# Kernel optimization log

Hardware: AMD Instinct MI355X
Metric: run time of the kernel (lower is better)

Reference implementation:

```python
import jax, jax.numpy as jnp
import numpy as np

HID = 256
HEADS = 4
NUM_GRAPHS = 8
NUM_RISK = 6

def _lstm_dir(x_pre, whh):
    # x_pre: [L, 4H] (input proj + both biases folded in), whh: [4H, H]
    Hh = whh.shape[1]
    def step(carry, xp):
        h, c = carry
        g = xp + whh @ h
        i, f, gg, o = jnp.split(g, 4)
        c = jax.nn.sigmoid(f) * c + jax.nn.sigmoid(i) * jnp.tanh(gg)
        h = jax.nn.sigmoid(o) * jnp.tanh(c)
        return (h, c), h
    init = (jnp.zeros((Hh,), x_pre.dtype), jnp.zeros((Hh,), x_pre.dtype))
    _, hs = jax.lax.scan(step, init, x_pre)
    return hs

def bilstm(x, wif, whf, bif, bhf, wir, whr, bir, bhr):
    pre_f = x @ wif.T + bif + bhf
    pre_r = x @ wir.T + bir + bhr
    hf = _lstm_dir(pre_f, whf)
    hb = _lstm_dir(pre_r[::-1], whr)[::-1]
    return jnp.concatenate([hf, hb], axis=-1)  # [N, 2H]

def gcn(h, src, dst, w, b, n):
    # PyG GCNConv: add self loops, symmetric deg^{-1/2} normalization
    xw = h @ w.T
    loop = jnp.arange(n, dtype=src.dtype)
    s = jnp.concatenate([src, loop]); d = jnp.concatenate([dst, loop])
    deg = jax.ops.segment_sum(jnp.ones_like(s, dtype=xw.dtype), d, num_segments=n)
    dinv = jax.lax.rsqrt(deg)  # deg >= 1 due to self loops
    coef = (dinv[s] * dinv[d])[:, None]
    return jax.ops.segment_sum(xw[s] * coef, d, num_segments=n) + b

def mha(h, in_w, in_b, out_w, out_b):
    # unbatched torch nn.MultiheadAttention, h: [L, E]
    L, E = h.shape
    hd = E // HEADS
    q, k, v = jnp.split(h @ in_w.T + in_b, 3, axis=-1)
    sp = lambda t: t.reshape(L, HEADS, hd).transpose(1, 0, 2)  # [H, L, hd]
    q, k, v = sp(q), sp(k), sp(v)
    a = jax.nn.softmax(jnp.einsum('hld,hmd->hlm', q, k) / np.sqrt(hd).astype(np.float32), axis=-1)
    o = jnp.einsum('hlm,hmd->hld', a, v).transpose(1, 0, 2).reshape(L, E)
    return o @ out_w.T + out_b

def ln(x, g, b, eps=1e-5):
    m = x.mean(-1, keepdims=True)
    v = ((x - m) ** 2).mean(-1, keepdims=True)
    return (x - m) * jax.lax.rsqrt(v + eps) * g + b

def setup_inputs() -> dict:
    key = jax.random.key(0)
    ks = iter(jax.random.split(key, 48))
    def nrm(shape, s=0.02):
        return jax.random.normal(next(ks), shape, dtype=jnp.float32) * s
    N, D, E, B, C, H = 3072, 768, 49152, NUM_GRAPHS, NUM_RISK, HID
    inp = {}
    inp['x'] = jax.random.normal(next(ks), (N, D), dtype=jnp.float32)
    inp['edge_index'] = jax.random.randint(next(ks), (2, E), 0, N, dtype=jnp.int32)
    inp['batch'] = jnp.sort(jax.random.randint(next(ks), (N,), 0, B, dtype=jnp.int32))
    # bidirectional LSTM (torch gate order i,f,g,o)
    inp['lstm_wif'] = nrm((4 * H, D)); inp['lstm_whf'] = nrm((4 * H, H))
    inp['lstm_bif'] = nrm((4 * H,));   inp['lstm_bhf'] = nrm((4 * H,))
    inp['lstm_wir'] = nrm((4 * H, D)); inp['lstm_whr'] = nrm((4 * H, H))
    inp['lstm_bir'] = nrm((4 * H,));   inp['lstm_bhr'] = nrm((4 * H,))
    # GCN layers (conv3 exists but is unused in forward)
    inp['gcn1_w'] = nrm((H, 2 * H)); inp['gcn1_b'] = nrm((H,))
    inp['gcn2_w'] = nrm((H, H));     inp['gcn2_b'] = nrm((H,))
    # per-risk-category attention / gate / predictor, stacked over C=6
    inp['attn_in_w'] = nrm((C, 3 * H, H)); inp['attn_in_b'] = nrm((C, 3 * H))
    inp['attn_out_w'] = nrm((C, H, H));    inp['attn_out_b'] = nrm((C, H))
    inp['gate_w1'] = nrm((C, H, 2 * H)); inp['gate_b1'] = nrm((C, H))
    inp['gate_w2'] = nrm((C, 1, H));     inp['gate_b2'] = nrm((C, 1))
    inp['pred_w1'] = nrm((C, 64, H)); inp['pred_b1'] = nrm((C, 64))
    inp['pred_w2'] = nrm((C, 1, 64)); inp['pred_b2'] = nrm((C, 1))
    # 2-layer post-LN TransformerEncoder, d_model=256, nhead=4, d_ff=2048
    inp['tr_in_w'] = nrm((2, 3 * H, H)); inp['tr_in_b'] = nrm((2, 3 * H))
    inp['tr_out_w'] = nrm((2, H, H));    inp['tr_out_b'] = nrm((2, H))
    inp['tr_ff1_w'] = nrm((2, 2048, H)); inp['tr_ff1_b'] = nrm((2, 2048))
    inp['tr_ff2_w'] = nrm((2, H, 2048)); inp['tr_ff2_b'] = nrm((2, H))
    inp['tr_ln1_g'] = jnp.ones((2, H), jnp.float32); inp['tr_ln1_b'] = nrm((2, H))
    inp['tr_ln2_g'] = jnp.ones((2, H), jnp.float32); inp['tr_ln2_b'] = nrm((2, H))
    return inp

def reference(x, edge_index, batch,
              lstm_wif, lstm_whf, lstm_bif, lstm_bhf,
              lstm_wir, lstm_whr, lstm_bir, lstm_bhr,
              gcn1_w, gcn1_b, gcn2_w, gcn2_b,
              attn_in_w, attn_in_b, attn_out_w, attn_out_b,
              gate_w1, gate_b1, gate_w2, gate_b2,
              pred_w1, pred_b1, pred_w2, pred_b2,
              tr_in_w, tr_in_b, tr_out_w, tr_out_b,
              tr_ff1_w, tr_ff1_b, tr_ff2_w, tr_ff2_b,
              tr_ln1_g, tr_ln1_b, tr_ln2_g, tr_ln2_b):
    N = x.shape[0]
    B = NUM_GRAPHS
    h = bilstm(x, lstm_wif, lstm_whf, lstm_bif, lstm_bhf,
               lstm_wir, lstm_whr, lstm_bir, lstm_bhr)  # [N, 512]
    src, dst = edge_index[0], edge_index[1]
    h = jax.nn.relu(gcn(h, src, dst, gcn1_w, gcn1_b, N))  # dropout is identity in eval
    h = jax.nn.relu(gcn(h, src, dst, gcn2_w, gcn2_b, N))  # [N, 256]
    counts = jnp.clip(jax.ops.segment_sum(jnp.ones((N,), h.dtype), batch, num_segments=B), 1.0)[:, None]
    scores, pooled_list = [], []
    for i in range(NUM_RISK):
        att = mha(h, attn_in_w[i], attn_in_b[i], attn_out_w[i], attn_out_b[i])
        g = jax.nn.sigmoid(jax.nn.relu(jnp.concatenate([h, att], -1) @ gate_w1[i].T + gate_b1[i]) @ gate_w2[i].T + gate_b2[i])
        prop = h + g * att
        pooled = jax.ops.segment_sum(prop, batch, num_segments=B) / counts  # [B, 256]
        sc = jax.nn.sigmoid(jax.nn.relu(pooled @ pred_w1[i].T + pred_b1[i]) @ pred_w2[i].T + pred_b2[i])
        scores.append(sc)
        pooled_list.append(pooled)
    s = jnp.stack(pooled_list, axis=1)  # [B, 6, 256]: torch treats axis0=seq, axis1=batch
    mha_b = jax.vmap(mha, in_axes=(1, None, None, None, None), out_axes=1)
    for l in range(2):  # post-LN TransformerEncoderLayer
        sa = mha_b(s, tr_in_w[l], tr_in_b[l], tr_out_w[l], tr_out_b[l])
        s = ln(s + sa, tr_ln1_g[l], tr_ln1_b[l])
        ff = jax.nn.relu(s @ tr_ff1_w[l].T + tr_ff1_b[l]) @ tr_ff2_w[l].T + tr_ff2_b[l]
        s = ln(s + ff, tr_ln2_g[l], tr_ln2_b[l])
    factor = jax.nn.sigmoid(s.mean(-1, keepdims=True))  # [B, 6, 1]
    out = jnp.stack([scores[i] * (1.0 + 0.2 * factor[:, i, :]) for i in range(NUM_RISK)], axis=0)
    return out  # [6, B, 1]
```

## Files before the change

kernel.cpp:

```cpp
#include <hip/hip_runtime.h>
#include <stdint.h>

typedef unsigned short u16;
typedef unsigned int   u32;
typedef __bf16    bf16x8 __attribute__((ext_vector_type(8)));
typedef float     f32x4  __attribute__((ext_vector_type(4)));
typedef _Float16  f16x2  __attribute__((ext_vector_type(2)));

#define DEV __device__ __forceinline__
#define MFMA16(a,b,c) __builtin_amdgcn_mfma_f32_16x16x32_bf16((a),(b),(c),0,0,0)
#define FDOT2(w,h,a) __builtin_amdgcn_fdot2(__builtin_bit_cast(f16x2,(w)), __builtin_bit_cast(f16x2,(h)), (a), false)

DEV u16  f2bf(float f){ u32 u = __builtin_bit_cast(u32,f); u32 r = (u + 0x7FFFu + ((u>>16)&1u))>>16; return (u16)r; }
DEV float bf2f(u16 b){ u32 u = ((u32)b)<<16; return __builtin_bit_cast(float,u); }
DEV u32  pkf16(float a, float b){ f16x2 p; p.x=(_Float16)a; p.y=(_Float16)b; return __builtin_bit_cast(u32,p); }
DEV u32  pkbf(float a, float b){ u32 r; asm("v_cvt_pk_bf16_f32 %0, %1, %2" : "=v"(r) : "v"(a), "v"(b)); return r; }
DEV float sigm(float x){ return 1.f/(1.f + exp2f(-1.44269504f*x)); }
DEV float tanh_(float x){ x = fminf(fmaxf(x,-15.f),15.f); float e = exp2f(2.88539008f*x); return (e-1.f)/(e+1.f); }

DEV void gl16(const u16* g, u16* l){
  __builtin_amdgcn_global_load_lds((const __attribute__((address_space(1))) void*)g,
                                   (__attribute__((address_space(3))) void*)l, 16, 0, 0);
}

__global__ void k_setup(int* cnt, int* fill, int* bstart, int* bend,
                        float* bias_pre, const float* bif, const float* bhf,
                        const float* bir, const float* bhr, float* pacc){
  int i = blockIdx.x*blockDim.x + threadIdx.x;
  if (i < 3072){ cnt[i]=0; fill[i]=0; }
  if (i < 1024){ bias_pre[i] = bif[i]+bhf[i]; bias_pre[1024+i] = bir[i]+bhr[i]; }
  if (i < 8){ bstart[i]=0; bend[i]=0; }
  if (i < 12288) pacc[i] = 0.f;
}

struct Cvt { const float* s[8]; u16* d[8]; int n[8]; };
__global__ void k_convert(Cvt c){
  for (int seg=0; seg<8; seg++){
    int n4 = c.n[seg]>>2;
    for (int i = blockIdx.x*blockDim.x+threadIdx.x; i < n4; i += gridDim.x*blockDim.x){
      float4 v = ((const float4*)c.s[seg])[i];
      uint2 o; o.x = (u32)f2bf(v.x) | ((u32)f2bf(v.y)<<16);
      o.y = (u32)f2bf(v.z) | ((u32)f2bf(v.w)<<16);
      *(uint2*)(c.d[seg] + (size_t)i*4) = o;
    }
  }
}

template<bool BF16OUT, bool RELU>
__global__ __launch_bounds__(256) void k_gemm(
  const u16* __restrict__ A, const u16* __restrict__ A2, const u16* __restrict__ B,
  const float* __restrict__ bias, void* __restrict__ Cout,
  int M, int N, int K1, int K2,
  long long sA, long long sA2, long long sB, long long sBias, long long sC)
{
  __shared__ __align__(16) u16 lA[128*32];
  __shared__ __align__(16) u16 lB[128*32];
  int bm = blockIdx.x, bn = blockIdx.y, bz = blockIdx.z;
  int tid = threadIdx.x, w = tid>>6, lane = tid&63;
  int wm = w&1, wn = w>>1;
  int m15 = lane&15, q = lane>>4;
  int srow = tid>>2, scol = (tid&3)*8;
  int K = K1+K2;
  f32x4 acc[4][4] = {};
  const u16* Ab  = A + (long long)bz*sA;
  const u16* A2b = A2 ? (A2 + (long long)bz*sA2) : (const u16*)0;
  const u16* Bb  = B + (long long)bz*sB;
  for (int k0 = 0; k0 < K; k0 += 32){
    uint4 av0, av1, bv0, bv1;
    if (k0 < K1){
      av0 = *(const uint4*)(Ab + (long long)(bm*128+srow   )*K1 + k0 + scol);
      av1 = *(const uint4*)(Ab + (long long)(bm*128+srow+64)*K1 + k0 + scol);
    } else {
      av0 = *(const uint4*)(A2b + (long long)(bm*128+srow   )*K2 + (k0-K1) + scol);
      av1 = *(const uint4*)(A2b + (long long)(bm*128+srow+64)*K2 + (k0-K1) + scol);
    }
    bv0 = *(const uint4*)(Bb + (long long)(bn*128+srow   )*K + k0 + scol);
    bv1 = *(const uint4*)(Bb + (long long)(bn*128+srow+64)*K + k0 + scol);
    __syncthreads();
    *(uint4*)&lA[(srow   )*32 + scol] = av0;
    *(uint4*)&lA[(srow+64)*32 + scol] = av1;
    *(uint4*)&lB[(srow   )*32 + scol] = bv0;
    *(uint4*)&lB[(srow+64)*32 + scol] = bv1;
    __syncthreads();
    bf16x8 af[4], bf[4];
    #pragma unroll
    for (int i=0;i<4;i++) af[i] = *(const bf16x8*)&lA[(wm*64+i*16+m15)*32 + q*8];
    #pragma unroll
    for (int j=0;j<4;j++) bf[j] = *(const bf16x8*)&lB[(wn*64+j*16+m15)*32 + q*8];
    #pragma unroll
    for (int i=0;i<4;i++){
      #pragma unroll
      for (int j=0;j<4;j++) acc[i][j] = MFMA16(af[i], bf[j], acc[i][j]);
    }
  }
  #pragma unroll
  for (int j=0;j<4;j++){
    int n = bn*128 + wn*64 + j*16 + m15;
    float bvv = bias ? bias[bz*sBias + n] : 0.f;
    #pragma unroll
    for (int i=0;i<4;i++){
      #pragma unroll
      for (int r=0;r<4;r++){
        int m = bm*128 + wm*64 + i*16 + q*4 + r;
        float v = acc[i][j][r] + bvv;
        if (RELU) v = fmaxf(v, 0.f);
        long long idx = (long long)bz*sC + (long long)m*N + n;
        if (BF16OUT) ((u16*)Cout)[idx] = f2bf(v);
        else         ((float*)Cout)[idx] = v;
      }
    }
  }
}

#define LSEG 24
#define LWARM 48
__global__ __launch_bounds__(512)
void k_lstm(
  const float* __restrict__ pre_all,
  const float* __restrict__ whf, const float* __restrict__ whr,
  u16* __restrict__ h_out)
{
  int bid = blockIdx.x;
  int dir = bid & 1, chunk = bid >> 1;
  int t = threadIdx.x;
  int d0 = t, d1 = t + 512;
  const float* pre = pre_all + (size_t)dir*3072*1024;
  const float* whh = dir ? whr : whf;

  __shared__ __align__(16) u32 wl[1024*28];
  __shared__ __align__(16) u32 hp[128];
  __shared__ float acts_f[256], acts_o[256];
  __shared__ float harr[256];

  u32 wr0[100], wr1[100];
  {
    const float* r0 = whh + (size_t)d0*256;
    const float* r1 = whh + (size_t)d1*256;
    #pragma unroll
    for (int p=0;p<50;p++){
      float4 w4 = *(const float4*)(r0 + 4*p);
      wr0[2*p]   = pkf16(w4.x, w4.y);
      wr0[2*p+1] = pkf16(w4.z, w4.w);
    }
    #pragma unroll
    for (int p=0;p<50;p++){
      float4 w4 = *(const float4*)(r1 + 4*p);
      wr1[2*p]   = pkf16(w4.x, w4.y);
      wr1[2*p+1] = pkf16(w4.z, w4.w);
    }
    #pragma unroll
    for (int p=0;p<14;p++){
      float4 w4 = *(const float4*)(r0 + 200 + 4*p);
      wl[d0*28 + 2*p]   = pkf16(w4.x, w4.y);
      wl[d0*28 + 2*p+1] = pkf16(w4.z, w4.w);
      float4 v4 = *(const float4*)(r1 + 200 + 4*p);
      wl[d1*28 + 2*p]   = pkf16(v4.x, v4.y);
      wl[d1*28 + 2*p+1] = pkf16(v4.z, v4.w);
    }
  }
  if (t < 128) hp[t] = 0u;
  __syncthreads();

  float c = 0.f;
  int warm = min(chunk*LSEG, LWARM);
  int nsteps = warm + LSEG;
  int s0 = chunk*LSEG - warm;
  const uint4* hp4 = (const uint4*)hp;
  const uint4* wl0 = (const uint4*)&wl[d0*28];
  const uint4* wl1 = (const uint4*)&wl[d1*28];
  for (int it = 0; it < nsteps; it++){
    int s = s0 + it;
    int n = dir ? (3071 - s) : s;
    float pv0 = pre[(size_t)n*1024 + d0];
    float pv1 = pre[(size_t)n*1024 + d1];
    float a00=0.f,a01=0.f,a10=0.f,a11=0.f;
    #pragma unroll
    for (int j=0;j<25;j++){
      uint4 h4 = hp4[j];
      a00 = FDOT2(wr0[4*j+0], h4.x, a00);
      a01 = FDOT2(wr0[4*j+1], h4.y, a01);
      a00 = FDOT2(wr0[4*j+2], h4.z, a00);
      a01 = FDOT2(wr0[4*j+3], h4.w, a01);
      a10 = FDOT2(wr1[4*j+0], h4.x, a10);
      a11 = FDOT2(wr1[4*j+1], h4.y, a11);
      a10 = FDOT2(wr1[4*j+2], h4.z, a10);
      a11 = FDOT2(wr1[4*j+3], h4.w, a11);
      __builtin_amdgcn_sched_barrier(0);
    }
    #pragma unroll
    for (int j=0;j<7;j++){
      uint4 h4 = hp4[25+j];
      uint4 w0 = wl0[j];
      uint4 w1 = wl1[j];
      a00 = FDOT2(w0.x, h4.x, a00);
      a01 = FDOT2(w0.y, h4.y, a01);
      a00 = FDOT2(w0.z, h4.z, a00);
      a01 = FDOT2(w0.w, h4.w, a01);
      a10 = FDOT2(w1.x, h4.x, a10);
      a11 = FDOT2(w1.y, h4.y, a11);
      a10 = FDOT2(w1.z, h4.z, a10);
      a11 = FDOT2(w1.w, h4.w, a11);
      __builtin_amdgcn_sched_barrier(0);
    }
    float gv0 = a00 + a01 + pv0;
    float gv1 = a10 + a11 + pv1;
    if (t >= 256){ acts_f[t-256] = sigm(gv0); acts_o[t-256] = sigm(gv1); }
    __syncthreads();
    if (t < 256){
      float ai = sigm(gv0), ag = tanh_(gv1);
      c = acts_f[t]*c + ai*ag;
      harr[t] = acts_o[t]*tanh_(c);
    }
    __syncthreads();
    if (t < 128){
      float h0 = harr[2*t], h1 = harr[2*t+1];
      hp[t] = pkf16(h0, h1);
      if (it >= warm){
        u32 pb = (u32)f2bf(h0) | ((u32)f2bf(h1) << 16);
        *(u32*)&h_out[(size_t)n*512 + dir*256 + 2*t] = pb;
      }
    }
    __syncthreads();
  }
}

__global__ void k_edge_cnt(const int* __restrict__ dst, int* __restrict__ cnt){
  int i = blockIdx.x*blockDim.x + threadIdx.x;
  if (i < 49152) atomicAdd(&cnt[dst[i]], 1);
}
__global__ __launch_bounds__(1024) void k_scan(const int* __restrict__ cnt, int* __restrict__ rowptr, float* __restrict__ dinv){
  __shared__ int lds[1024];
  int t = threadIdx.x;
  int a0 = cnt[t*3], a1 = cnt[t*3+1], a2 = cnt[t*3+2];
  int s = a0+a1+a2;
  lds[t] = s; __syncthreads();
  for (int off=1; off<1024; off<<=1){
    int v = (t>=off) ? lds[t-off] : 0; __syncthreads();
    lds[t] += v; __syncthreads();
  }
  int base = lds[t] - s;
  rowptr[t*3] = base; rowptr[t*3+1] = base+a0; rowptr[t*3+2] = base+a0+a1;
  if (t == 1023) rowptr[3072] = base + s;
  dinv[t*3]   = rsqrtf((float)(a0+1));
  dinv[t*3+1] = rsqrtf((float)(a1+1));
  dinv[t*3+2] = rsqrtf((float)(a2+1));
}
__global__ void k_fill(const int* __restrict__ src, const int* __restrict__ dst,
                       const int* __restrict__ rowptr, int* __restrict__ fill, int* __restrict__ csrc){
  int i = blockIdx.x*blockDim.x + threadIdx.x;
  if (i < 49152){ int d = dst[i]; int pos = rowptr[d] + atomicAdd(&fill[d],1); csrc[pos] = src[i]; }
}

__global__ __launch_bounds__(256) void k_gcn_agg(const float* __restrict__ xw, const int* __restrict__ rowptr,
  const int* __restrict__ csrc, const float* __restrict__ dinv, const float* __restrict__ bias,
  float* __restrict__ outf, u16* __restrict__ outb){
  int wv = threadIdx.x>>6, lane = threadIdx.x&63;
  int dst = blockIdx.x*4 + wv;
  float dd = dinv[dst];
  int beg = rowptr[dst], end = rowptr[dst+1];
  const float4* x4 = (const float4*)xw;
  float4 acc = {0.f,0.f,0.f,0.f};
  for (int e=beg;e<end;e++){
    int s = csrc[e];
    float cf = dd*dinv[s];
    float4 v = x4[(size_t)s*64 + lane];
    acc.x += cf*v.x; acc.y += cf*v.y; acc.z += cf*v.z; acc.w += cf*v.w;
  }
  { float cf = dd*dd; float4 v = x4[(size_t)dst*64+lane];
    acc.x += cf*v.x; acc.y += cf*v.y; acc.z += cf*v.z; acc.w += cf*v.w; }
  float4 bb = ((const float4*)bias)[lane];
  acc.x = fmaxf(acc.x+bb.x,0.f); acc.y = fmaxf(acc.y+bb.y,0.f);
  acc.z = fmaxf(acc.z+bb.z,0.f); acc.w = fmaxf(acc.w+bb.w,0.f);
  if (outf) ((float4*)outf)[(size_t)dst*64+lane] = acc;
  uint2 o; o.x = (u32)f2bf(acc.x) | ((u32)f2bf(acc.y)<<16);
  o.y = (u32)f2bf(acc.z) | ((u32)f2bf(acc.w)<<16);
  *(uint2*)&outb[(size_t)dst*256 + lane*4] = o;
}

__global__ void k_bounds(const int* __restrict__ batch, int* __restrict__ bstart, int* __restrict__ bend){
  int n = blockIdx.x*blockDim.x+threadIdx.x;
  if (n>=3072) return;
  int b = batch[n];
  if (n==0 || batch[n-1]!=b) bstart[b]=n;
  if (n==3071 || batch[n+1]!=b) bend[b]=n+1;
}

__global__ __launch_bounds__(256) void k_vt(const u16* __restrict__ qkv, u16* __restrict__ vT){
  int p = blockIdx.x, nt = blockIdx.y;
  int risk = p >> 2, hd = p & 3;
  __shared__ u16 t[64][72];
  int r = threadIdx.x >> 2, ch = threadIdx.x & 3;
  const u16* src = qkv + (size_t)risk*3072*768 + (size_t)(nt*64 + r)*768 + 512 + hd*64 + ch*16;
  uint4 v0 = *(const uint4*)src;
  uint4 v1 = *(const uint4*)(src+8);
  *(uint4*)&t[r][ch*16] = v0; *(uint4*)&t[r][ch*16+8] = v1;
  __syncthreads();
  int d = threadIdx.x >> 2, nc = threadIdx.x & 3;
  u16 tmp[16];
  #pragma unroll
  for (int j=0;j<16;j++) tmp[j] = t[nc*16 + j][d];
  u32 a0 = (u32)tmp[0] | ((u32)tmp[1]<<16), a1 = (u32)tmp[2] | ((u32)tmp[3]<<16);
  u32 a2 = (u32)tmp[4] | ((u32)tmp[5]<<16), a3 = (u32)tmp[6] | ((u32)tmp[7]<<16);
  u32 a4 = (u32)tmp[8] | ((u32)tmp[9]<<16), a5 = (u32)tmp[10]| ((u32)tmp[11]<<16);
  u32 a6 = (u32)tmp[12]| ((u32)tmp[13]<<16),a7 = (u32)tmp[14]| ((u32)tmp[15]<<16);
  u16* dstp = vT + (size_t)p*64*3072 + (size_t)d*3072 + nt*64 + nc*16;
  uint4 o1 = {a0,a1,a2,a3}; uint4 o2 = {a4,a5,a6,a7};
  *(uint4*)dstp = o1; *(uint4*)(dstp+8) = o2;
}

#define KSW(r,c) (((r)<<6) + ((((c)^((r)&7)))<<3))
__global__ __launch_bounds__(256) void k_flash(const u16* __restrict__ qkv, const u16* __restrict__ vT,
                                               u16* __restrict__ outO){
  int qt = blockIdx.x;
  int pair = blockIdx.y;
  int risk = pair>>2, hd = pair&3;
  int tid = threadIdx.x, w = tid>>6, lane = tid&63;
  int m = lane&15, q = lane>>4;
  __shared__ __align__(16) u16 lK[2][64*64];
  __shared__ __align__(16) u16 lV[2][64*64];
  __shared__ __align__(16) u16 lP[4*16*72];
  const size_t qbase = (size_t)risk*3072*768;
  bf16x8 aq0, aq1;
  {
    const u16* qp = qkv + qbase + (size_t)(qt*64 + w*16 + m)*768 + hd*64 + q*8;
    aq0 = *(const bf16x8*)qp; aq1 = *(const bf16x8*)(qp+32);
  }
  f32x4 o[4] = {};
  f32x4 lrow = {};
  const u16* kg = qkv + qbase + 256 + hd*64;
  const u16* vg = vT + (size_t)pair*64*3072;
  int sro = lane>>3;
  int sch = (lane&7) ^ sro;
  int wbase = w*16*72;
  const float SC = 0.18033688f;
  #pragma unroll
  for (int i=0;i<2;i++){
    int row = w*16 + i*8 + sro;
    gl16(kg + (size_t)row*768 + sch*8,  &lK[0][(w*16+i*8)*64]);
    gl16(vg + (size_t)row*3072 + sch*8, &lV[0][(w*16+i*8)*64]);
  }
  __syncthreads();
  int cur = 0;
  for (int kt=0; kt<48; kt++){
    if (kt < 47){
      int nb = cur^1;
      #pragma unroll
      for (int i=0;i<2;i++){
        int row = w*16 + i*8 + sro;
        gl16(kg + (size_t)((kt+1)*64 + row)*768 + sch*8,   &lK[nb][(w*16+i*8)*64]);
        gl16(vg + (size_t)row*3072 + (kt+1)*64 + sch*8,    &lV[nb][(w*16+i*8)*64]);
      }
    }
    #pragma unroll
    for (int j=0;j<4;j++){
      bf16x8 b0 = *(const bf16x8*)&lK[cur][KSW(j*16+m, q)];
      bf16x8 b1 = *(const bf16x8*)&lK[cur][KSW(j*16+m, q+4)];
      f32x4 cfr = {};
      cfr = MFMA16(aq0, b0, cfr);
      cfr = MFMA16(aq1, b1, cfr);
      float pe[4];
      #pragma unroll
      for (int r=0;r<4;r++){
        pe[r] = exp2f(cfr[r]*SC);
        lrow[r] += pe[r];
      }
      #pragma unroll
      for (int r=0;r<4;r++){
        float po = __shfl_xor(pe[r],1);
        if (!(lane&1)){
          *(u32*)&lP[wbase + (q*4+r)*72 + j*16 + m] = pkbf(pe[r], po);
        }
      }
    }
    bf16x8 ap0 = *(const bf16x8*)&lP[wbase + m*72 + q*8];
    bf16x8 ap1 = *(const bf16x8*)&lP[wbase + m*72 + 32 + q*8];
    #pragma unroll
    for (int jd=0;jd<4;jd++){
      bf16x8 b0 = *(const bf16x8*)&lV[cur][KSW(jd*16+m, q)];
      bf16x8 b1 = *(const bf16x8*)&lV[cur][KSW(jd*16+m, q+4)];
      o[jd] = MFMA16(ap0, b0, o[jd]);
      o[jd] = MFMA16(ap1, b1, o[jd]);
    }
    __syncthreads();
    cur ^= 1;
  }
  float rl[4];
  #pragma unroll
  for (int r=0;r<4;r++){
    float s = lrow[r];
    #pragma unroll
    for (int sh=1; sh<16; sh<<=1) s += __shfl_xor(s, sh);
    rl[r] = 1.f/s;
  }
  #pragma unroll
  for (int jd=0;jd<4;jd++){
    #pragma unroll
    for (int r=0;r<4;r++){
      float v = o[jd][r]*rl[r];
      float vo = __shfl_xor(v,1);
      if (!(lane&1)){
        int row = qt*64 + w*16 + q*4 + r;
        *(u32*)&outO[((size_t)risk*3072 + row)*256 + hd*64 + jd*16 + m] = pkbf(v, vo);
      }
    }
  }
}

__global__ __launch_bounds__(256) void k_gate2(const u16* __restrict__ gh, const float* __restrict__ w2,
    const float* __restrict__ b2, float* __restrict__ g){
  int wv = threadIdx.x>>6, lane = threadIdx.x&63;
  int row = blockIdx.x*4 + wv;
  int i = row / 3072;
  const u16* rp = gh + (size_t)row*256 + lane*4;
  uint2 d = *(const uint2*)rp;
  float4 wv4 = *(const float4*)(w2 + i*256 + lane*4);
  float p = bf2f((u16)(d.x&0xffff))*wv4.x + bf2f((u16)(d.x>>16))*wv4.y
          + bf2f((u16)(d.y&0xffff))*wv4.z + bf2f((u16)(d.y>>16))*wv4.w;
  #pragma unroll
  for (int sh=1;sh<64;sh<<=1) p += __shfl_xor(p, sh);
  if (lane==0) g[row] = sigm(p + b2[i]);
}

__global__ __launch_bounds__(256) void k_pool(const float* __restrict__ hf, const u16* __restrict__ att,
  const float* __restrict__ g, const int* __restrict__ bstart, const int* __restrict__ bend,
  float* __restrict__ pacc){
  int i = blockIdx.x/8, b = blockIdx.x%8, d = threadIdx.x;
  int beg = bstart[b], end = bend[b];
  int len = end - beg;
  int c0 = beg + (int)(((long long)len*blockIdx.y)>>2);
  int c1 = beg + (int)(((long long)len*(blockIdx.y+1))>>2);
  float acc = 0.f;
  for (int n=c0;n<c1;n++)
    acc += hf[(size_t)n*256 + d] + g[i*3072+n]*bf2f(att[((size_t)i*3072+n)*256 + d]);
  atomicAdd(&pacc[(size_t)blockIdx.x*256 + d], acc);
}
__global__ __launch_bounds__(256) void k_poolfin(const float* __restrict__ pacc,
  const int* __restrict__ bstart, const int* __restrict__ bend,
  float* __restrict__ pooled, float* __restrict__ sbuf){
  int i = blockIdx.x/8, b = blockIdx.x%8, d = threadIdx.x;
  float cnt = fmaxf((float)(bend[b]-bstart[b]), 1.f);
  float pv = pacc[(size_t)blockIdx.x*256 + d]/cnt;
  pooled[(size_t)blockIdx.x*256 + d] = pv;
  sbuf[(size_t)(b*6+i)*256 + d] = pv;
}

__global__ __launch_bounds__(64) void k_pred(const float* __restrict__ pooled, const float* __restrict__ w1,
  const float* __restrict__ b1, const float* __restrict__ w2, const float* __restrict__ b2,
  float* __restrict__ sc){
  int i = blockIdx.x/8, j = threadIdx.x;
  const float* p = pooled + (size_t)blockIdx.x*256;
  const float* wr = w1 + ((size_t)i*64 + j)*256;
  float acc = 0.f;
  for (int k=0;k<256;k+=4){
    float4 a=*(const float4*)(p+k); float4 wv=*(const float4*)(wr+k);
    acc += a.x*wv.x+a.y*wv.y+a.z*wv.z+a.w*wv.w;
  }
  float h = fmaxf(acc + b1[i*64+j], 0.f);
  float part = h * w2[i*64+j];
  #pragma unroll
  for (int sh=1;sh<64;sh<<=1) part += __shfl_xor(part, sh);
  if (j==0) sc[blockIdx.x] = sigm(part + b2[i]);
}

DEV float blksum256(float v, float* red){
  #pragma unroll
  for (int sh=1;sh<64;sh<<=1) v += __shfl_xor(v,sh);
  int wv = threadIdx.x>>6;
  if ((threadIdx.x&63)==0) red[wv]=v;
  __syncthreads();
  float r = red[0]+red[1]+red[2]+red[3];
  __syncthreads();
  return r;
}
__global__ __launch_bounds__(256) void k_tqkv(const float* __restrict__ sbuf, const float* __restrict__ w,
  const float* __restrict__ bias, float* __restrict__ qkvt){
  int bi = blockIdx.x;
  __shared__ float sv[256];
  sv[threadIdx.x] = sbuf[bi*256 + threadIdx.x];
  __syncthreads();
  for (int r=0;r<3;r++){
    int row = r*256 + threadIdx.x;
    const float* wr = w + (size_t)row*256;
    float acc=0.f;
    for (int k=0;k<256;k+=4){
      float4 wv=*(const float4*)(wr+k);
      acc += sv[k]*wv.x + sv[k+1]*wv.y + sv[k+2]*wv.z + sv[k+3]*wv.w;
    }
    qkvt[(size_t)bi*768 + row] = acc + bias[row];
  }
}
__global__ __launch_bounds__(64) void k_tattn(const float* __restrict__ qkvt, float* __restrict__ attt){
  int i = blockIdx.x>>2, hd = blockIdx.x&3, d = threadIdx.x;
  __shared__ float q[8][64], k[8][64], v[8][64], p[8][8];
  for (int a=0;a<8;a++){
    const float* bp = qkvt + (size_t)(a*6+i)*768 + hd*64 + d;
    q[a][d] = bp[0]; k[a][d] = bp[256]; v[a][d] = bp[512];
  }
  __syncthreads();
  {
    int a = d>>3, b2 = d&7;
    float s = 0.f;
    for (int kk=0; kk<64; kk++) s += q[a][kk]*k[b2][kk];
    s *= 0.125f;
    float mx = s;
    #pragma unroll
    for (int sh=1;sh<8;sh<<=1) mx = fmaxf(mx, __shfl_xor(mx,sh));
    float e = exp2f((s-mx)*1.44269504f);
    float sum = e;
    #pragma unroll
    for (int sh=1;sh<8;sh<<=1) sum += __shfl_xor(sum,sh);
    p[a][b2] = e/sum;
  }
  __syncthreads();
  for (int a=0;a<8;a++){
    float acc=0.f;
    #pragma unroll
    for (int b2=0;b2<8;b2++) acc += p[a][b2]*v[b2][d];
    attt[(size_t)(a*6+i)*256 + hd*64 + d] = acc;
  }
}
__global__ __launch_bounds__(256) void k_tout(const float* __restrict__ attt, const float* __restrict__ w,
  const float* __restrict__ bias, const float* __restrict__ lng, const float* __restrict__ lnb,
  float* __restrict__ sbuf){
  int bi = blockIdx.x, t = threadIdx.x;
  __shared__ float av[256]; __shared__ float red[4];
  av[t] = attt[bi*256+t]; __syncthreads();
  const float* wr = w + (size_t)t*256;
  float acc=0.f;
  for (int k=0;k<256;k+=4){
    float4 wv=*(const float4*)(wr+k);
    acc += av[k]*wv.x + av[k+1]*wv.y + av[k+2]*wv.z + av[k+3]*wv.w;
  }
  float x = sbuf[bi*256+t] + acc + bias[t];
  float mean = blksum256(x, red)/256.f;
  float dd = x-mean;
  float var = blksum256(dd*dd, red)/256.f;
  sbuf[bi*256+t] = dd*rsqrtf(var+1e-5f)*lng[t] + lnb[t];
}
__global__ __launch_bounds__(256) void k_tff1(const float* __restrict__ sbuf, const float* __restrict__ w,
  const float* __restrict__ bias, float* __restrict__ ff1){
  int bi = blockIdx.x, j = blockIdx.y*256 + threadIdx.x;
  __shared__ float sv[256];
  sv[threadIdx.x] = sbuf[bi*256+threadIdx.x]; __syncthreads();
  const float* wr = w + (size_t)j*256;
  float acc=0.f;
  for (int k=0;k<256;k+=4){
    float4 wv=*(const float4*)(wr+k);
    acc += sv[k]*wv.x + sv[k+1]*wv.y + sv[k+2]*wv.z + sv[k+3]*wv.w;
  }
  ff1[(size_t)bi*2048 + j] = fmaxf(acc + bias[j], 0.f);
}
__global__ __launch_bounds__(256) void k_tff2(const float* __restrict__ ff1, const float* __restrict__ w,
  const float* __restrict__ bias, const float* __restrict__ lng, const float* __restrict__ lnb,
  float* __restrict__ sbuf){
  int bi = blockIdx.x, t = threadIdx.x;
  __shared__ float lff[2048]; __shared__ float red[4];
  for (int j=t;j<2048;j+=256) lff[j] = ff1[(size_t)bi*2048 + j];
  __syncthreads();
  const float* wr = w + (size_t)t*2048;
  float acc = 0.f;
  for (int k=0;k<2048;k+=4){
    float4 wv=*(const float4*)(wr+k);
    acc += lff[k]*wv.x + lff[k+1]*wv.y + lff[k+2]*wv.z + lff[k+3]*wv.w;
  }
  float x = sbuf[bi*256+t] + acc + bias[t];
  float mean = blksum256(x, red)/256.f;
  float dd = x-mean;
  float var = blksum256(dd*dd, red)/256.f;
  sbuf[bi*256+t] = dd*rsqrtf(var+1e-5f)*lng[t] + lnb[t];
}
__global__ __launch_bounds__(64) void k_final(const float* __restrict__ sbuf, const float* __restrict__ sc,
  float* __restrict__ out){
  int i = blockIdx.x/8, b = blockIdx.x%8, t = threadIdx.x;
  const float* row = sbuf + (size_t)(b*6+i)*256;
  float v = row[t] + row[t+64] + row[t+128] + row[t+192];
  #pragma unroll
  for (int sh=1;sh<64;sh<<=1) v += __shfl_xor(v,sh);
  if (t==0){
    float factor = sigm(v/256.f);
    out[i*8+b] = sc[i*8+b]*(1.f + 0.2f*factor);
  }
}

extern "C" void kernel_launch(void* const* d_in, const int* in_sizes, int n_in,
                              void* d_out, int out_size, void* d_ws, size_t ws_size,
                              hipStream_t stream){
  (void)in_sizes; (void)n_in; (void)out_size; (void)ws_size;
  const float* x    = (const float*)d_in[0];
  const int* edge   = (const int*)d_in[1];
  const int* batch  = (const int*)d_in[2];
  const float* wif  = (const float*)d_in[3];
  const float* whf  = (const float*)d_in[4];
  const float* bif  = (const float*)d_in[5];
  const float* bhf  = (const float*)d_in[6];
  const float* wir  = (const float*)d_in[7];
  const float* whr  = (const float*)d_in[8];
  const float* bir  = (const float*)d_in[9];
  const float* bhr  = (const float*)d_in[10];
  const float* gcn1w = (const float*)d_in[11];
  const float* gcn1b = (const float*)d_in[12];
  const float* gcn2w = (const float*)d_in[13];
  const float* gcn2b = (const float*)d_in[14];
  const float* ainw  = (const float*)d_in[15];
  const float* ainb  = (const float*)d_in[16];
  const float* aoutw = (const float*)d_in[17];
  const float* aoutb = (const float*)d_in[18];
  const float* gw1   = (const float*)d_in[19];
  const float* gb1   = (const float*)d_in[20];
  const float* gw2   = (const float*)d_in[21];
  const float* gb2   = (const float*)d_in[22];
  const float* pw1   = (const float*)d_in[23];
  const float* pb1   = (const float*)d_in[24];
  const float* pw2   = (const float*)d_in[25];
  const float* pb2   = (const float*)d_in[26];
  const float* trinw = (const float*)d_in[27];
  const float* trinb = (const float*)d_in[28];
  const float* troutw= (const float*)d_in[29];
  const float* troutb= (const float*)d_in[30];
  const float* trff1w= (const float*)d_in[31];
  const float* trff1b= (const float*)d_in[32];
  const float* trff2w= (const float*)d_in[33];
  const float* trff2b= (const float*)d_in[34];
  const float* ln1g  = (const float*)d_in[35];
  const float* ln1b  = (const float*)d_in[36];
  const float* ln2g  = (const float*)d_in[37];
  const float* ln2b  = (const float*)d_in[38];

  char* base = (char*)d_ws; size_t off = 0;
  auto alloc = [&](size_t bytes)->void*{ void* p = base+off; off += (bytes+255)&~(size_t)255; return p; };
  float* pre      = (float*)alloc((size_t)2*3072*1024*4);
  u16* x_bf       = (u16*)alloc((size_t)3072*768*2);
  u16* wpre_bf    = (u16*)alloc((size_t)2*1024*768*2);
  float* bias_pre = (float*)alloc(2*1024*4);
  u16* hlstm_bf   = (u16*)alloc((size_t)3072*512*2);
  u16* g1w_bf     = (u16*)alloc(256*512*2);
  u16* g2w_bf     = (u16*)alloc(256*256*2);
  int* cnt        = (int*)alloc(3072*4);
  int* fill       = (int*)alloc(3072*4);
  int* rowptr     = (int*)alloc(3073*4);
  float* dinv     = (float*)alloc(3072*4);
  int* csrc       = (int*)alloc(49152*4);
  float* xw       = (float*)alloc((size_t)3072*256*4);
  u16* hg1_bf     = (u16*)alloc((size_t)3072*256*2);
  float* h_f32    = (float*)alloc((size_t)3072*256*4);
  u16* h_bf       = (u16*)alloc((size_t)3072*256*2);
  u16* ainw_bf    = (u16*)alloc((size_t)6*768*256*2);
  u16* aoutw_bf   = (u16*)alloc((size_t)6*256*256*2);
  u16* gw1_bf     = (u16*)alloc((size_t)6*256*512*2);
  u16* qkv_bf     = (u16*)alloc((size_t)6*3072*768*2);
  u16* vT         = (u16*)alloc((size_t)24*64*3072*2);
  u16* aO_bf      = (u16*)alloc((size_t)6*3072*256*2);
  u16* att_bf     = (u16*)alloc((size_t)6*3072*256*2);
  u16* gh_bf      = (u16*)alloc((size_t)6*3072*256*2);
  float* gvec     = (float*)alloc(6*3072*4);
  int* bstart     = (int*)alloc(8*4);
  int* bend       = (int*)alloc(8*4);
  float* pacc     = (float*)alloc(48*256*4);
  float* pooled   = (float*)alloc(48*256*4);
  float* sbuf     = (float*)alloc(48*256*4);
  float* scv      = (float*)alloc(48*4);
  float* qkvt     = (float*)alloc(48*768*4);
  float* attt     = (float*)alloc(48*256*4);
  float* ff1      = (float*)alloc(48*2048*4);

  k_setup<<<64,256,0,stream>>>(cnt, fill, bstart, bend, bias_pre, bif,bhf,bir,bhr, pacc);

  Cvt cv;
  cv.s[0]=x;     cv.d[0]=x_bf;              cv.n[0]=3072*768;
  cv.s[1]=wif;   cv.d[1]=wpre_bf;           cv.n[1]=1024*768;
  cv.s[2]=wir;   cv.d[2]=wpre_bf+1024*768;  cv.n[2]=1024*768;
  cv.s[3]=gcn1w; cv.d[3]=g1w_bf;            cv.n[3]=256*512;
  cv.s[4]=gcn2w; cv.d[4]=g2w_bf;            cv.n[4]=256*256;
  cv.s[5]=ainw;  cv.d[5]=ainw_bf;           cv.n[5]=6*768*256;
  cv.s[6]=aoutw; cv.d[6]=aoutw_bf;          cv.n[6]=6*256*256;
  cv.s[7]=gw1;   cv.d[7]=gw1_bf;            cv.n[7]=6*256*512;
  k_convert<<<512,256,0,stream>>>(cv);

  dim3 gpre(24,8,2);
  k_gemm<false,false><<<gpre,256,0,stream>>>(x_bf, nullptr, wpre_bf, bias_pre, pre,
      3072,1024,768,0, 0,0, (long long)1024*768, 1024, (long long)3072*1024);

  k_lstm<<<256,512,0,stream>>>(pre, whf, whr, hlstm_bf);

  k_edge_cnt<<<192,256,0,stream>>>(edge+49152, cnt);
  k_scan<<<1,1024,0,stream>>>(cnt, rowptr, dinv);
  k_fill<<<192,256,0,stream>>>(edge, edge+49152, rowptr, fill, csrc);

  dim3 gx1(24,2,1);
  k_gemm<false,false><<<gx1,256,0,stream>>>(hlstm_bf, nullptr, g1w_bf, nullptr, xw,
      3072,256,512,0, 0,0,0,0,0);
  k_gcn_agg<<<768,256,0,stream>>>(xw, rowptr, csrc, dinv, gcn1b, nullptr, hg1_bf);
  k_gemm<false,false><<<gx1,256,0,stream>>>(hg1_bf, nullptr, g2w_bf, nullptr, xw,
      3072,256,256,0, 0,0,0,0,0);
  k_gcn_agg<<<768,256,0,stream>>>(xw, rowptr, csrc, dinv, gcn2b, h_f32, h_bf);
  k_bounds<<<12,256,0,stream>>>(batch, bstart, bend);

  dim3 gq(24,6,6);
  k_gemm<true,false><<<gq,256,0,stream>>>(h_bf, nullptr, ainw_bf, ainb, qkv_bf,
      3072,768,256,0, 0,0, (long long)768*256, 768, (long long)3072*768);
  dim3 gvt(24,48);
  k_vt<<<gvt,256,0,stream>>>(qkv_bf, vT);
  dim3 gfl(48,24);
  k_flash<<<gfl,256,0,stream>>>(qkv_bf, vT, aO_bf);
  dim3 go(24,2,6);
  k_gemm<true,false><<<go,256,0,stream>>>(aO_bf, nullptr, aoutw_bf, aoutb, att_bf,
      3072,256,256,0, (long long)3072*256, 0, (long long)256*256, 256, (long long)3072*256);
  k_gemm<true,true><<<go,256,0,stream>>>(h_bf, att_bf, gw1_bf, gb1, gh_bf,
      3072,256,256,256, 0, (long long)3072*256, (long long)256*512, 256, (long long)3072*256);
  k_gate2<<<6*768,256,0,stream>>>(gh_bf, gw2, gb2, gvec);
  dim3 gp(48,4);
  k_pool<<<gp,256,0,stream>>>(h_f32, att_bf, gvec, bstart, bend, pacc);
  k_poolfin<<<48,256,0,stream>>>(pacc, bstart, bend, pooled, sbuf);
  k_pred<<<48,64,0,stream>>>(pooled, pw1, pb1, pw2, pb2, scv);

  for (int l=0;l<2;l++){
    k_tqkv<<<48,256,0,stream>>>(sbuf, trinw + (size_t)l*768*256, trinb + l*768, qkvt);
    k_tattn<<<24,64,0,stream>>>(qkvt, attt);
    k_tout<<<48,256,0,stream>>>(attt, troutw + (size_t)l*256*256, troutb + l*256,
                                ln1g + l*256, ln1b + l*256, sbuf);
    dim3 gff(48,8);
    k_tff1<<<gff,256,0,stream>>>(sbuf, trff1w + (size_t)l*2048*256, trff1b + l*2048, ff1);
    k_tff2<<<48,256,0,stream>>>(ff1, trff2w + (size_t)l*256*2048, trff2b + l*256,
                                ln2g + l*256, ln2b + l*256, sbuf);
  }
  k_final<<<48,64,0,stream>>>(sbuf, scv, (float*)d_out);
}
```

Baseline: 1.029 ms.

## Split flash attention over two KV halves and combine partials in a new kernel

The attention kernel now splits the 48 key tiles into two halves along a new grid z dimension. Each half writes unnormalized fp32 output partials and row sums. A new combine kernel adds the two halves, normalizes, and packs to bf16. This doubles the block count to cut tail-wave underutilization across CUs, at the cost of extra fp32 partial traffic and an additional launch. The plain sum of partials is only valid because the softmax uses no running max.

```diff
diff --git a/kernel.cpp b/kernel.cpp
--- a/kernel.cpp
+++ b/kernel.cpp
@@ -309,10 +309,12 @@
 }
 
 #define KSW(r,c) (((r)<<6) + ((((c)^((r)&7)))<<3))
+#define KH 24
 __global__ __launch_bounds__(256) void k_flash(const u16* __restrict__ qkv, const u16* __restrict__ vT,
-                                               u16* __restrict__ outO){
+                                               float* __restrict__ opart, float* __restrict__ lpart){
   int qt = blockIdx.x;
   int pair = blockIdx.y;
+  int half = blockIdx.z;
   int risk = pair>>2, hd = pair&3;
   int tid = threadIdx.x, w = tid>>6, lane = tid&63;
   int m = lane&15, q = lane>>4;
@@ -333,16 +335,17 @@
   int sch = (lane&7) ^ sro;
   int wbase = w*16*72;
   const float SC = 0.18033688f;
+  int kt0 = half*KH;
   #pragma unroll
   for (int i=0;i<2;i++){
     int row = w*16 + i*8 + sro;
-    gl16(kg + (size_t)row*768 + sch*8,  &lK[0][(w*16+i*8)*64]);
-    gl16(vg + (size_t)row*3072 + sch*8, &lV[0][(w*16+i*8)*64]);
+    gl16(kg + (size_t)(kt0*64 + row)*768 + sch*8,  &lK[0][(w*16+i*8)*64]);
+    gl16(vg + (size_t)row*3072 + kt0*64 + sch*8,   &lV[0][(w*16+i*8)*64]);
   }
   __syncthreads();
   int cur = 0;
-  for (int kt=0; kt<48; kt++){
-    if (kt < 47){
+  for (int kt=kt0; kt<kt0+KH; kt++){
+    if (kt < kt0+KH-1){
       int nb = cur^1;
       #pragma unroll
       for (int i=0;i<2;i++){
@@ -384,26 +387,37 @@
     __syncthreads();
     cur ^= 1;
   }
-  float rl[4];
   #pragma unroll
   for (int r=0;r<4;r++){
     float s = lrow[r];
     #pragma unroll
     for (int sh=1; sh<16; sh<<=1) s += __shfl_xor(s, sh);
-    rl[r] = 1.f/s;
+    if (m == 0){
+      int row = qt*64 + w*16 + q*4 + r;
+      lpart[(size_t)half*18432 + risk*3072 + row] = s;
+    }
   }
   #pragma unroll
   for (int jd=0;jd<4;jd++){
     #pragma unroll
     for (int r=0;r<4;r++){
-      float v = o[jd][r]*rl[r];
-      float vo = __shfl_xor(v,1);
-      if (!(lane&1)){
-        int row = qt*64 + w*16 + q*4 + r;
-        *(u32*)&outO[((size_t)risk*3072 + row)*256 + hd*64 + jd*16 + m] = pkbf(v, vo);
-      }
-    }
-  }
+      int row = qt*64 + w*16 + q*4 + r;
+      opart[((size_t)half*18432 + risk*3072 + row)*256 + hd*64 + jd*16 + m] = o[jd][r];
+    }
+  }
+}
+
+__global__ __launch_bounds__(256) void k_ocomb(const float* __restrict__ op, const float* __restrict__ lp,
+                                               u16* __restrict__ outO){
+  int rowg = blockIdx.x*4 + (threadIdx.x>>6);
+  int c4 = (threadIdx.x&63)*4;
+  float4 a = *(const float4*)&op[(size_t)rowg*256 + c4];
+  float4 b = *(const float4*)&op[((size_t)18432 + rowg)*256 + c4];
+  float li = 1.f/(lp[rowg] + lp[18432 + rowg]);
+  uint2 o;
+  o.x = pkbf((a.x+b.x)*li, (a.y+b.y)*li);
+  o.y = pkbf((a.z+b.z)*li, (a.w+b.w)*li);
+  *(uint2*)&outO[(size_t)rowg*256 + c4] = o;
 }
 
 __global__ __launch_bounds__(256) void k_gate2(const u16* __restrict__ gh, const float* __restrict__ w2,
@@ -649,6 +663,8 @@
   u16* gw1_bf     = (u16*)alloc((size_t)6*256*512*2);
   u16* qkv_bf     = (u16*)alloc((size_t)6*3072*768*2);
   u16* vT         = (u16*)alloc((size_t)24*64*3072*2);
+  float* opart    = (float*)alloc((size_t)2*18432*256*4);
+  float* lpart    = (float*)alloc((size_t)2*18432*4);
   u16* aO_bf      = (u16*)alloc((size_t)6*3072*256*2);
   u16* att_bf     = (u16*)alloc((size_t)6*3072*256*2);
   u16* gh_bf      = (u16*)alloc((size_t)6*3072*256*2);
@@ -700,8 +716,9 @@
       3072,768,256,0, 0,0, (long long)768*256, 768, (long long)3072*768);
   dim3 gvt(24,48);
   k_vt<<<gvt,256,0,stream>>>(qkv_bf, vT);
-  dim3 gfl(48,24);
-  k_flash<<<gfl,256,0,stream>>>(qkv_bf, vT, aO_bf);
+  dim3 gfl(48,24,2);
+  k_flash<<<gfl,256,0,stream>>>(qkv_bf, vT, opart, lpart);
+  k_ocomb<<<4608,256,0,stream>>>(opart, lpart, aO_bf);
   dim3 go(24,2,6);
   k_gemm<true,false><<<go,256,0,stream>>>(aO_bf, nullptr, aoutw_bf, aoutb, att_bf,
       3072,256,256,0, (long long)3072*256, 0, (long long)256*256, 256, (long long)3072*256);
```

Measured after the change: 1.012 ms. No clear change (-1.7%).
